# Kernel optimization log

Hardware: AMD Instinct MI355X
Metric: run time of the kernel (lower is better)

Reference implementation:

```python
import jax, jax.numpy as jnp
import numpy as np

N_NODES = 200000  # num_users + num_items
N_EDGES = 1000000
D = 64


def setup_inputs() -> dict:
    key = jax.random.key(0)
    ks = jax.random.split(key, 9)
    return {
        "src": jax.random.randint(ks[0], (N_EDGES,), 0, N_NODES, dtype=jnp.int32),
        "dst": jax.random.randint(ks[1], (N_EDGES,), 0, N_NODES, dtype=jnp.int32),
        "review_feat": jax.random.normal(ks[2], (N_EDGES, D), dtype=jnp.float32),
        "ci_r": jax.random.uniform(ks[3], (N_NODES, 1), dtype=jnp.float32),
        "feature": jax.random.normal(ks[4], (N_NODES, D), dtype=jnp.float32),
        "W1": jax.random.normal(ks[5], (D, D), dtype=jnp.float32) * 0.05,
        "W2": jax.random.normal(ks[6], (D, D), dtype=jnp.float32) * 0.05,
        "feature2": jax.random.normal(ks[7], (N_NODES, D), dtype=jnp.float32) * 0.05,
        "feature3": jax.random.normal(ks[8], (N_NODES, D), dtype=jnp.float32) * 0.05,
    }


def reference(src, dst, review_feat, ci_r, feature, W1, W2, feature2, feature3):
    # Eval-mode forward (is_training=False, freeze='', dropout = identity).
    # `feature` is assigned to g.srcdata['h_r'] in the original but never used.
    n = ci_r.shape[0]
    ci_src = ci_r[src]            # [E,1] gather of src norm coeff
    ci_dst = ci_r                 # [N,1]

    # Pass 1: edge linear on review features, scaled by src coeff, scatter-sum.
    r = review_feat @ W1.T                                   # [E,64]
    h1 = jax.ops.segment_sum(r * ci_src, dst, num_segments=n)
    rst_re = h1 * ci_dst

    # Pass 2: (src embedding + edge transform) messages.
    r_fe = review_feat @ W2.T                                # [E,64]
    m2 = (feature2[src] + r_fe) * ci_src
    h2 = jax.ops.segment_sum(m2, dst, num_segments=n)
    rst = h2 * ci_dst

    # Pass 3: pure src-embedding messages.
    m3 = feature3[src] * ci_src
    h3 = jax.ops.segment_sum(m3, dst, num_segments=n)
    rst_id = h3 * ci_dst

    return (rst, rst_re, rst_id)
```

## Files before the change

### kernel.cpp

```cpp
#include <hip/hip_runtime.h>

#define NN 200000
#define NE 1000000
#define DD 64
#define NCHUNK 196

typedef __bf16 bf16x4 __attribute__((ext_vector_type(4)));
typedef __bf16 bf16x8 __attribute__((ext_vector_type(8)));
typedef float  f32x4  __attribute__((ext_vector_type(4)));

static __device__ __forceinline__ bf16x8 pack8(const float* __restrict__ p) {
    float4 a = *reinterpret_cast<const float4*>(p);
    float4 b = *reinterpret_cast<const float4*>(p + 4);
    bf16x8 r;
    r[0] = (__bf16)a.x; r[1] = (__bf16)a.y; r[2] = (__bf16)a.z; r[3] = (__bf16)a.w;
    r[4] = (__bf16)b.x; r[5] = (__bf16)b.y; r[6] = (__bf16)b.z; r[7] = (__bf16)b.w;
    return r;
}

static __device__ __forceinline__ bf16x8 pack8s(const float* __restrict__ p, float c) {
    float4 a = *reinterpret_cast<const float4*>(p);
    float4 b = *reinterpret_cast<const float4*>(p + 4);
    bf16x8 r;
    r[0] = (__bf16)(a.x * c); r[1] = (__bf16)(a.y * c);
    r[2] = (__bf16)(a.z * c); r[3] = (__bf16)(a.w * c);
    r[4] = (__bf16)(b.x * c); r[5] = (__bf16)(b.y * c);
    r[6] = (__bf16)(b.z * c); r[7] = (__bf16)(b.w * c);
    return r;
}

__global__ __launch_bounds__(256) void k_prep(
    const int* __restrict__ dst, const float* __restrict__ f2,
    const float* __restrict__ f3, const float* __restrict__ ci,
    int* __restrict__ counts, __bf16* __restrict__ f2c, __bf16* __restrict__ f3c)
{
    const int b = blockIdx.x;
    if (b < 1024) {
        for (int e = b * 256 + threadIdx.x; e < NE; e += 1024 * 256)
            atomicAdd(&counts[dst[e]], 1);
    } else {
        const size_t per = (size_t)NN * DD / 8;
        const size_t stride = (size_t)(gridDim.x - 1024) * 256;
        for (size_t i = (size_t)(b - 1024) * 256 + threadIdx.x; i < per; i += stride) {
            const int row = (int)(i >> 3);
            const float c = ci[row];
            *reinterpret_cast<bf16x8*>(f2c + i * 8) = pack8s(f2 + i * 8, c);
            *reinterpret_cast<bf16x8*>(f3c + i * 8) = pack8s(f3 + i * 8, c);
        }
    }
}

__global__ __launch_bounds__(256) void k_chunk_sums(const int* __restrict__ counts,
                                                    int* __restrict__ csum) {
    const int b = blockIdx.x, tid = threadIdx.x;
    const int base = b * 1024 + tid * 4;
    int s = 0;
#pragma unroll
    for (int j = 0; j < 4; ++j) {
        const int i = base + j;
        if (i < NN) s += counts[i];
    }
#pragma unroll
    for (int d = 32; d > 0; d >>= 1) s += __shfl_down(s, d);
    __shared__ int wsum[4];
    if ((tid & 63) == 0) wsum[tid >> 6] = s;
    __syncthreads();
    if (tid == 0) csum[b] = wsum[0] + wsum[1] + wsum[2] + wsum[3];
}

__global__ void k_scan_chunks(const int* __restrict__ csum, int* __restrict__ cofs) {
    if (threadIdx.x == 0 && blockIdx.x == 0) {
        int acc = 0;
        for (int i = 0; i < NCHUNK; ++i) { cofs[i] = acc; acc += csum[i]; }
    }
}

__global__ __launch_bounds__(256) void k_chunk_scan(const int* __restrict__ counts,
                                                    const int* __restrict__ cofs,
                                                    int* __restrict__ offs,
                                                    int* __restrict__ cursor) {
    const int b = blockIdx.x, tid = threadIdx.x;
    const int lane = tid & 63, wv = tid >> 6;
    const int base = b * 1024 + tid * 4;
    int c[4];
#pragma unroll
    for (int j = 0; j < 4; ++j) {
        const int i = base + j;
        c[j] = (i < NN) ? counts[i] : 0;
    }
    const int ls = c[0] + c[1] + c[2] + c[3];
    int v = ls;
#pragma unroll
    for (int d = 1; d < 64; d <<= 1) {
        const int u = __shfl_up(v, d);
        if (lane >= d) v += u;
    }
    __shared__ int wsum[4];
    if (lane == 63) wsum[wv] = v;
    __syncthreads();
    int wbase = 0;
    for (int w = 0; w < wv; ++w) wbase += wsum[w];
    int excl = cofs[b] + wbase + (v - ls);
#pragma unroll
    for (int j = 0; j < 4; ++j) {
        const int i = base + j;
        if (i < NN) { offs[i] = excl; cursor[i] = excl; }
        excl += c[j];
    }
}

__global__ __launch_bounds__(256) void k_permfill_msg(
    const int* __restrict__ dst, const int* __restrict__ src,
    const float* __restrict__ ci, const float* __restrict__ review,
    int* __restrict__ cursor, __bf16* __restrict__ mrev, int* __restrict__ srcs)
{
    const int tid = threadIdx.x;
    const int l16 = tid & 15;
    const int e   = blockIdx.x * 16 + (tid >> 4);

    const int s = src[e];
    const float cs = ci[s];
    int pos = 0;
    if (l16 == 0) pos = atomicAdd(&cursor[dst[e]], 1);
    pos = __shfl(pos, tid & 48);

    const float4 r = *reinterpret_cast<const float4*>(review + (size_t)e * DD + l16 * 4);
    bf16x4 m;
    m[0] = (__bf16)(r.x * cs); m[1] = (__bf16)(r.y * cs);
    m[2] = (__bf16)(r.z * cs); m[3] = (__bf16)(r.w * cs);
    *reinterpret_cast<bf16x4*>(mrev + (size_t)pos * DD + l16 * 4) = m;
    if (l16 == 0) srcs[pos] = s;
}

__global__ __launch_bounds__(256) void k_pull_fused(
    const __bf16* __restrict__ mrev, const int* __restrict__ srcs,
    const int* __restrict__ offs, const int* __restrict__ counts,
    const float* __restrict__ ci,
    const __bf16* __restrict__ f2c, const __bf16* __restrict__ f3c,
    const float* __restrict__ W1, const float* __restrict__ W2,
    float* __restrict__ out_rst, float* __restrict__ out_re,
    float* __restrict__ out_id)
{
    __shared__ __bf16 At[16][64];
    __shared__ float  S2[16][64];

    const int tid = threadIdx.x;
    const int l16 = tid & 15;
    const int q   = tid >> 4;
    const int n   = blockIdx.x * 16 + q;

    const int beg = offs[n];
    const int cnt = counts[n];

    float4 ax0 = {0,0,0,0}, a20 = {0,0,0,0}, a30 = {0,0,0,0};
    float4 ax1 = {0,0,0,0}, a21 = {0,0,0,0}, a31 = {0,0,0,0};

    int k = 0;
    for (; k + 2 <= cnt; k += 2) {
        const int sa = srcs[beg + k];
        const int sb = srcs[beg + k + 1];
        const bf16x4 ma = *reinterpret_cast<const bf16x4*>(mrev + (size_t)(beg + k) * DD + l16 * 4);
        const bf16x4 mb = *reinterpret_cast<const bf16x4*>(mrev + (size_t)(beg + k + 1) * DD + l16 * 4);
        const bf16x4 p2a = *reinterpret_cast<const bf16x4*>(f2c + (size_t)sa * DD + l16 * 4);
        const bf16x4 p2b = *reinterpret_cast<const bf16x4*>(f2c + (size_t)sb * DD + l16 * 4);
        const bf16x4 p3a = *reinterpret_cast<const bf16x4*>(f3c + (size_t)sa * DD + l16 * 4);
        const bf16x4 p3b = *reinterpret_cast<const bf16x4*>(f3c + (size_t)sb * DD + l16 * 4);
        ax0.x += (float)ma[0]; ax0.y += (float)ma[1];
        ax0.z += (float)ma[2]; ax0.w += (float)ma[3];
        ax1.x += (float)mb[0]; ax1.y += (float)mb[1];
        ax1.z += (float)mb[2]; ax1.w += (float)mb[3];
        a20.x += (float)p2a[0]; a20.y += (float)p2a[1];
        a20.z += (float)p2a[2]; a20.w += (float)p2a[3];
        a21.x += (float)p2b[0]; a21.y += (float)p2b[1];
        a21.z += (float)p2b[2]; a21.w += (float)p2b[3];
        a30.x += (float)p3a[0]; a30.y += (float)p3a[1];
        a30.z += (float)p3a[2]; a30.w += (float)p3a[3];
        a31.x += (float)p3b[0]; a31.y += (float)p3b[1];
        a31.z += (float)p3b[2]; a31.w += (float)p3b[3];
    }
    if (k < cnt) {
        const int sa = srcs[beg + k];
        const bf16x4 ma = *reinterpret_cast<const bf16x4*>(mrev + (size_t)(beg + k) * DD + l16 * 4);
        const bf16x4 p2a = *reinterpret_cast<const bf16x4*>(f2c + (size_t)sa * DD + l16 * 4);
        const bf16x4 p3a = *reinterpret_cast<const bf16x4*>(f3c + (size_t)sa * DD + l16 * 4);
        ax0.x += (float)ma[0]; ax0.y += (float)ma[1];
        ax0.z += (float)ma[2]; ax0.w += (float)ma[3];
        a20.x += (float)p2a[0]; a20.y += (float)p2a[1];
        a20.z += (float)p2a[2]; a20.w += (float)p2a[3];
        a30.x += (float)p3a[0]; a30.y += (float)p3a[1];
        a30.z += (float)p3a[2]; a30.w += (float)p3a[3];
    }

    const float cid = ci[n];
    float4 ax = {ax0.x + ax1.x, ax0.y + ax1.y, ax0.z + ax1.z, ax0.w + ax1.w};
    float4 a2 = {a20.x + a21.x, a20.y + a21.y, a20.z + a21.z, a20.w + a21.w};
    float4 a3 = {a30.x + a31.x, a30.y + a31.y, a30.z + a31.z, a30.w + a31.w};

    float4 v3 = {a3.x * cid, a3.y * cid, a3.z * cid, a3.w * cid};
    *reinterpret_cast<float4*>(out_id + (size_t)n * DD + l16 * 4) = v3;

    bf16x4 hb;
    hb[0] = (__bf16)(ax.x * cid); hb[1] = (__bf16)(ax.y * cid);
    hb[2] = (__bf16)(ax.z * cid); hb[3] = (__bf16)(ax.w * cid);
    *reinterpret_cast<bf16x4*>(&At[q][l16 * 4]) = hb;
    float4 s2v = {a2.x * cid, a2.y * cid, a2.z * cid, a2.w * cid};
    *reinterpret_cast<float4*>(&S2[q][l16 * 4]) = s2v;
    __syncthreads();

    const int w  = tid >> 6;
    const int lq = (tid & 63) >> 4;
    bf16x8 w1f[2], w2f[2];
#pragma unroll
    for (int kk = 0; kk < 2; ++kk) {
        const int off = (w * 16 + l16) * DD + kk * 32 + lq * 8;
        w1f[kk] = pack8(W1 + off);
        w2f[kk] = pack8(W2 + off);
    }
    const bf16x8 a0 = *reinterpret_cast<const bf16x8*>(&At[l16][lq * 8]);
    const bf16x8 a1 = *reinterpret_cast<const bf16x8*>(&At[l16][lq * 8 + 32]);

    const f32x4 zero = {0.f, 0.f, 0.f, 0.f};
    f32x4 acc1 = zero, acc2 = zero;
    acc1 = __builtin_amdgcn_mfma_f32_16x16x32_bf16(a0, w1f[0], acc1, 0, 0, 0);
    acc1 = __builtin_amdgcn_mfma_f32_16x16x32_bf16(a1, w1f[1], acc1, 0, 0, 0);
    acc2 = __builtin_amdgcn_mfma_f32_16x16x32_bf16(a0, w2f[0], acc2, 0, 0, 0);
    acc2 = __builtin_amdgcn_mfma_f32_16x16x32_bf16(a1, w2f[1], acc2, 0, 0, 0);

    const int base = blockIdx.x * 16;
#pragma unroll
    for (int i = 0; i < 4; ++i) {
        const int row = lq * 4 + i;
        const size_t o = (size_t)(base + row) * DD + w * 16 + l16;
        out_re[o]  = acc1[i];
        out_rst[o] = acc2[i] + S2[row][w * 16 + l16];
    }
}

__global__ __launch_bounds__(256) void gcn_mfma_kernel(
    const int* __restrict__ src, const int* __restrict__ dst,
    const float* __restrict__ review, const float* __restrict__ ci,
    const float* __restrict__ W1, const float* __restrict__ W2,
    const float* __restrict__ f2, const float* __restrict__ f3,
    float* __restrict__ out)
{
    float* out_rst = out;
    float* out_re  = out + (size_t)NN * DD;
    float* out_id  = out + 2 * (size_t)NN * DD;
    const int lane = threadIdx.x & 63;
    const int l16  = lane & 15;
    const int lq   = lane >> 4;
    const int wid  = blockIdx.x * (blockDim.x >> 6) + (threadIdx.x >> 6);
    const int nw   = gridDim.x * (blockDim.x >> 6);

    bf16x8 w1f[4][2], w2f[4][2];
#pragma unroll
    for (int c = 0; c < 4; ++c)
#pragma unroll
        for (int kk = 0; kk < 2; ++kk) {
            const int off = (c * 16 + l16) * DD + kk * 32 + lq * 8;
            w1f[c][kk] = pack8(W1 + off);
            w2f[c][kk] = pack8(W2 + off);
        }
    const f32x4 zero = {0.f, 0.f, 0.f, 0.f};
    for (int t = wid; t < NE / 16; t += nw) {
        const int e0 = t * 16;
        const float* xr = review + (size_t)(e0 + l16) * DD + lq * 8;
        const bf16x8 a0 = pack8(xr);
        const bf16x8 a1 = pack8(xr + 32);
        f32x4 acc1[4], acc2[4];
#pragma unroll
        for (int c = 0; c < 4; ++c) { acc1[c] = zero; acc2[c] = zero; }
#pragma unroll
        for (int c = 0; c < 4; ++c) {
            acc1[c] = __builtin_amdgcn_mfma_f32_16x16x32_bf16(a0, w1f[c][0], acc1[c], 0, 0, 0);
            acc1[c] = __builtin_amdgcn_mfma_f32_16x16x32_bf16(a1, w1f[c][1], acc1[c], 0, 0, 0);
            acc2[c] = __builtin_amdgcn_mfma_f32_16x16x32_bf16(a0, w2f[c][0], acc2[c], 0, 0, 0);
            acc2[c] = __builtin_amdgcn_mfma_f32_16x16x32_bf16(a1, w2f[c][1], acc2[c], 0, 0, 0);
        }
        int sA[4], dA[4]; float cf[4];
#pragma unroll
        for (int i = 0; i < 4; ++i) {
            const int e = e0 + lq * 4 + i;
            sA[i] = src[e]; dA[i] = dst[e];
            cf[i] = ci[sA[i]] * ci[dA[i]];
        }
#pragma unroll
        for (int i = 0; i < 4; ++i) {
            const size_t so = (size_t)sA[i] * DD;
            const size_t dofs = (size_t)dA[i] * DD;
            const float c_ = cf[i];
#pragma unroll
            for (int c = 0; c < 4; ++c) {
                const int col = c * 16 + l16;
                atomicAdd(out_re  + dofs + col, acc1[c][i] * c_);
                atomicAdd(out_rst + dofs + col, (f2[so + col] + acc2[c][i]) * c_);
                atomicAdd(out_id  + dofs + col, f3[so + col] * c_);
            }
        }
    }
}

extern "C" void kernel_launch(void* const* d_in, const int* in_sizes, int n_in,
                              void* d_out, int out_size, void* d_ws, size_t ws_size,
                              hipStream_t stream) {
    const int*   src    = (const int*)d_in[0];
    const int*   dst    = (const int*)d_in[1];
    const float* review = (const float*)d_in[2];
    const float* ci     = (const float*)d_in[3];
    const float* W1     = (const float*)d_in[5];
    const float* W2     = (const float*)d_in[6];
    const float* f2     = (const float*)d_in[7];
    const float* f3     = (const float*)d_in[8];
    float* out = (float*)d_out;
    float* out_rst = out;
    float* out_re  = out + (size_t)NN * DD;
    float* out_id  = out + 2 * (size_t)NN * DD;

    const size_t NEED = sizeof(int) * ((size_t)3 * NN + 512 + NE) +
                        2 * sizeof(__bf16) * (size_t)NN * DD +
                        sizeof(__bf16) * (size_t)NE * DD;
    if (ws_size < NEED) {
        hipMemsetAsync(out, 0, (size_t)out_size * sizeof(float), stream);
        gcn_mfma_kernel<<<2048, 256, 0, stream>>>(src, dst, review, ci, W1, W2, f2, f3, out);
        return;
    }

    char* w = (char*)d_ws;
    int* counts = (int*)w;    w += (size_t)NN * 4;
    int* offs   = (int*)w;    w += (size_t)NN * 4;
    int* cursor = (int*)w;    w += (size_t)NN * 4;
    int* csum   = (int*)w;    w += 256 * 4;
    int* cofs   = (int*)w;    w += 256 * 4;
    int* srcs   = (int*)w;    w += (size_t)NE * 4;
    __bf16* f2c = (__bf16*)w; w += (size_t)NN * DD * 2;
    __bf16* f3c = (__bf16*)w; w += (size_t)NN * DD * 2;
    __bf16* mrev = (__bf16*)w;

    hipMemsetAsync(counts, 0, (size_t)NN * 4, stream);
    k_prep        <<<3072, 256, 0, stream>>>(dst, f2, f3, ci, counts, f2c, f3c);
    k_chunk_sums  <<<NCHUNK, 256, 0, stream>>>(counts, csum);
    k_scan_chunks <<<1, 64, 0, stream>>>(csum, cofs);
    k_chunk_scan  <<<NCHUNK, 256, 0, stream>>>(counts, cofs, offs, cursor);
    k_permfill_msg<<<NE / 16, 256, 0, stream>>>(dst, src, ci, review, cursor, mrev, srcs);
    k_pull_fused  <<<NN / 16, 256, 0, stream>>>(mrev, srcs, offs, counts, ci,
                                                f2c, f3c, W1, W2,
                                                out_rst, out_re, out_id);
}
```

Before: 318.3 us.

## Drop bf16 pre-scaled feature copies and gather fp32 features with per-edge coeff

Removes the prep pass that converted feature2/feature3 to ci-scaled bf16 copies. The pull kernel now gathers fp32 rows directly and applies the source coefficient, which is stored next to the src index as an int2 per sorted edge. The memset is replaced by a small zero kernel and the histogram gets its own kernel. This saves writing and reading the 2x25.6MB bf16 copies, but the random gathers in the pull kernel now move twice as many bytes per row and also read the coefficient per edge.

Measured after the change: 316.1 us. About the same (-0.7%).

```diff
diff --git a/kernel.cpp b/kernel.cpp
--- a/kernel.cpp
+++ b/kernel.cpp
@@ -18,36 +18,20 @@
     return r;
 }
 
-static __device__ __forceinline__ bf16x8 pack8s(const float* __restrict__ p, float c) {
-    float4 a = *reinterpret_cast<const float4*>(p);
-    float4 b = *reinterpret_cast<const float4*>(p + 4);
-    bf16x8 r;
-    r[0] = (__bf16)(a.x * c); r[1] = (__bf16)(a.y * c);
-    r[2] = (__bf16)(a.z * c); r[3] = (__bf16)(a.w * c);
-    r[4] = (__bf16)(b.x * c); r[5] = (__bf16)(b.y * c);
-    r[6] = (__bf16)(b.z * c); r[7] = (__bf16)(b.w * c);
-    return r;
-}
-
-__global__ __launch_bounds__(256) void k_prep(
-    const int* __restrict__ dst, const float* __restrict__ f2,
-    const float* __restrict__ f3, const float* __restrict__ ci,
-    int* __restrict__ counts, __bf16* __restrict__ f2c, __bf16* __restrict__ f3c)
-{
-    const int b = blockIdx.x;
-    if (b < 1024) {
-        for (int e = b * 256 + threadIdx.x; e < NE; e += 1024 * 256)
-            atomicAdd(&counts[dst[e]], 1);
+__global__ __launch_bounds__(256) void k_zero(int* __restrict__ counts) {
+    const int i = (blockIdx.x * 256 + threadIdx.x) * 4;
+    if (i + 3 < NN) {
+        *reinterpret_cast<int4*>(counts + i) = make_int4(0, 0, 0, 0);
     } else {
-        const size_t per = (size_t)NN * DD / 8;
-        const size_t stride = (size_t)(gridDim.x - 1024) * 256;
-        for (size_t i = (size_t)(b - 1024) * 256 + threadIdx.x; i < per; i += stride) {
-            const int row = (int)(i >> 3);
-            const float c = ci[row];
-            *reinterpret_cast<bf16x8*>(f2c + i * 8) = pack8s(f2 + i * 8, c);
-            *reinterpret_cast<bf16x8*>(f3c + i * 8) = pack8s(f3 + i * 8, c);
-        }
-    }
+        for (int j = i; j < NN; ++j) counts[j] = 0;
+    }
+}
+
+__global__ __launch_bounds__(256) void k_hist(const int* __restrict__ dst,
+                                              int* __restrict__ counts) {
+    for (int e = blockIdx.x * blockDim.x + threadIdx.x; e < NE;
+         e += gridDim.x * blockDim.x)
+        atomicAdd(&counts[dst[e]], 1);
 }
 
 __global__ __launch_bounds__(256) void k_chunk_sums(const int* __restrict__ counts,
@@ -112,7 +96,7 @@
 __global__ __launch_bounds__(256) void k_permfill_msg(
     const int* __restrict__ dst, const int* __restrict__ src,
     const float* __restrict__ ci, const float* __restrict__ review,
-    int* __restrict__ cursor, __bf16* __restrict__ mrev, int* __restrict__ srcs)
+    int* __restrict__ cursor, __bf16* __restrict__ mrev, int2* __restrict__ esrc)
 {
     const int tid = threadIdx.x;
     const int l16 = tid & 15;
@@ -129,14 +113,14 @@
     m[0] = (__bf16)(r.x * cs); m[1] = (__bf16)(r.y * cs);
     m[2] = (__bf16)(r.z * cs); m[3] = (__bf16)(r.w * cs);
     *reinterpret_cast<bf16x4*>(mrev + (size_t)pos * DD + l16 * 4) = m;
-    if (l16 == 0) srcs[pos] = s;
+    if (l16 == 0) esrc[pos] = make_int2(s, __float_as_int(cs));
 }
 
 __global__ __launch_bounds__(256) void k_pull_fused(
-    const __bf16* __restrict__ mrev, const int* __restrict__ srcs,
+    const __bf16* __restrict__ mrev, const int2* __restrict__ esrc,
     const int* __restrict__ offs, const int* __restrict__ counts,
     const float* __restrict__ ci,
-    const __bf16* __restrict__ f2c, const __bf16* __restrict__ f3c,
+    const float* __restrict__ f2, const float* __restrict__ f3,
     const float* __restrict__ W1, const float* __restrict__ W2,
     float* __restrict__ out_rst, float* __restrict__ out_re,
     float* __restrict__ out_id)
@@ -157,38 +141,41 @@
 
     int k = 0;
     for (; k + 2 <= cnt; k += 2) {
-        const int sa = srcs[beg + k];
-        const int sb = srcs[beg + k + 1];
+        const int2 ea = esrc[beg + k];
+        const int2 eb = esrc[beg + k + 1];
+        const float ca = __int_as_float(ea.y);
+        const float cb = __int_as_float(eb.y);
         const bf16x4 ma = *reinterpret_cast<const bf16x4*>(mrev + (size_t)(beg + k) * DD + l16 * 4);
         const bf16x4 mb = *reinterpret_cast<const bf16x4*>(mrev + (size_t)(beg + k + 1) * DD + l16 * 4);
-        const bf16x4 p2a = *reinterpret_cast<const bf16x4*>(f2c + (size_t)sa * DD + l16 * 4);
-        const bf16x4 p2b = *reinterpret_cast<const bf16x4*>(f2c + (size_t)sb * DD + l16 * 4);
-        const bf16x4 p3a = *reinterpret_cast<const bf16x4*>(f3c + (size_t)sa * DD + l16 * 4);
-        const bf16x4 p3b = *reinterpret_cast<const bf16x4*>(f3c + (size_t)sb * DD + l16 * 4);
+        const float4 p2a = *reinterpret_cast<const float4*>(f2 + (size_t)ea.x * DD + l16 * 4);
+        const float4 p2b = *reinterpret_cast<const float4*>(f2 + (size_t)eb.x * DD + l16 * 4);
+        const float4 p3a = *reinterpret_cast<const float4*>(f3 + (size_t)ea.x * DD + l16 * 4);
+        const float4 p3b = *reinterpret_cast<const float4*>(f3 + (size_t)eb.x * DD + l16 * 4);
         ax0.x += (float)ma[0]; ax0.y += (float)ma[1];
         ax0.z += (float)ma[2]; ax0.w += (float)ma[3];
         ax1.x += (float)mb[0]; ax1.y += (float)mb[1];
         ax1.z += (float)mb[2]; ax1.w += (float)mb[3];
-        a20.x += (float)p2a[0]; a20.y += (float)p2a[1];
-        a20.z += (float)p2a[2]; a20.w += (float)p2a[3];
-        a21.x += (float)p2b[0]; a21.y += (float)p2b[1];
-        a21.z += (float)p2b[2]; a21.w += (float)p2b[3];
-        a30.x += (float)p3a[0]; a30.y += (float)p3a[1];
-        a30.z += (float)p3a[2]; a30.w += (float)p3a[3];
-        a31.x += (float)p3b[0]; a31.y += (float)p3b[1];
-        a31.z += (float)p3b[2]; a31.w += (float)p3b[3];
+        a20.x = fmaf(p2a.x, ca, a20.x); a20.y = fmaf(p2a.y, ca, a20.y);
+        a20.z = fmaf(p2a.z, ca, a20.z); a20.w = fmaf(p2a.w, ca, a20.w);
+        a21.x = fmaf(p2b.x, cb, a21.x); a21.y = fmaf(p2b.y, cb, a21.y);
+        a21.z = fmaf(p2b.z, cb, a21.z); a21.w = fmaf(p2b.w, cb, a21.w);
+        a30.x = fmaf(p3a.x, ca, a30.x); a30.y = fmaf(p3a.y, ca, a30.y);
+        a30.z = fmaf(p3a.z, ca, a30.z); a30.w = fmaf(p3a.w, ca, a30.w);
+        a31.x = fmaf(p3b.x, cb, a31.x); a31.y = fmaf(p3b.y, cb, a31.y);
+        a31.z = fmaf(p3b.z, cb, a31.z); a31.w = fmaf(p3b.w, cb, a31.w);
     }
     if (k < cnt) {
-        const int sa = srcs[beg + k];
+        const int2 ea = esrc[beg + k];
+        const float ca = __int_as_float(ea.y);
         const bf16x4 ma = *reinterpret_cast<const bf16x4*>(mrev + (size_t)(beg + k) * DD + l16 * 4);
-        const bf16x4 p2a = *reinterpret_cast<const bf16x4*>(f2c + (size_t)sa * DD + l16 * 4);
-        const bf16x4 p3a = *reinterpret_cast<const bf16x4*>(f3c + (size_t)sa * DD + l16 * 4);
+        const float4 p2a = *reinterpret_cast<const float4*>(f2 + (size_t)ea.x * DD + l16 * 4);
+        const float4 p3a = *reinterpret_cast<const float4*>(f3 + (size_t)ea.x * DD + l16 * 4);
         ax0.x += (float)ma[0]; ax0.y += (float)ma[1];
         ax0.z += (float)ma[2]; ax0.w += (float)ma[3];
-        a20.x += (float)p2a[0]; a20.y += (float)p2a[1];
-        a20.z += (float)p2a[2]; a20.w += (float)p2a[3];
-        a30.x += (float)p3a[0]; a30.y += (float)p3a[1];
-        a30.z += (float)p3a[2]; a30.w += (float)p3a[3];
+        a20.x = fmaf(p2a.x, ca, a20.x); a20.y = fmaf(p2a.y, ca, a20.y);
+        a20.z = fmaf(p2a.z, ca, a20.z); a20.w = fmaf(p2a.w, ca, a20.w);
+        a30.x = fmaf(p3a.x, ca, a30.x); a30.y = fmaf(p3a.y, ca, a30.y);
+        a30.z = fmaf(p3a.z, ca, a30.z); a30.w = fmaf(p3a.w, ca, a30.w);
     }
 
     const float cid = ci[n];
@@ -316,8 +303,8 @@
     float* out_re  = out + (size_t)NN * DD;
     float* out_id  = out + 2 * (size_t)NN * DD;
 
-    const size_t NEED = sizeof(int) * ((size_t)3 * NN + 512 + NE) +
-                        2 * sizeof(__bf16) * (size_t)NN * DD +
+    const size_t NEED = sizeof(int) * ((size_t)3 * NN + 512) +
+                        sizeof(int2) * (size_t)NE +
                         sizeof(__bf16) * (size_t)NE * DD;
     if (ws_size < NEED) {
         hipMemsetAsync(out, 0, (size_t)out_size * sizeof(float), stream);
@@ -331,18 +318,16 @@
     int* cursor = (int*)w;    w += (size_t)NN * 4;
     int* csum   = (int*)w;    w += 256 * 4;
     int* cofs   = (int*)w;    w += 256 * 4;
-    int* srcs   = (int*)w;    w += (size_t)NE * 4;
-    __bf16* f2c = (__bf16*)w; w += (size_t)NN * DD * 2;
-    __bf16* f3c = (__bf16*)w; w += (size_t)NN * DD * 2;
+    int2* esrc  = (int2*)w;   w += (size_t)NE * 8;
     __bf16* mrev = (__bf16*)w;
 
-    hipMemsetAsync(counts, 0, (size_t)NN * 4, stream);
-    k_prep        <<<3072, 256, 0, stream>>>(dst, f2, f3, ci, counts, f2c, f3c);
+    k_zero        <<<(NN / 4 + 255) / 256, 256, 0, stream>>>(counts);
+    k_hist        <<<1024, 256, 0, stream>>>(dst, counts);
     k_chunk_sums  <<<NCHUNK, 256, 0, stream>>>(counts, csum);
     k_scan_chunks <<<1, 64, 0, stream>>>(csum, cofs);
     k_chunk_scan  <<<NCHUNK, 256, 0, stream>>>(counts, cofs, offs, cursor);
-    k_permfill_msg<<<NE / 16, 256, 0, stream>>>(dst, src, ci, review, cursor, mrev, srcs);
-    k_pull_fused  <<<NN / 16, 256, 0, stream>>>(mrev, srcs, offs, counts, ci,
-                                                f2c, f3c, W1, W2,
+    k_permfill_msg<<<NE / 16, 256, 0, stream>>>(dst, src, ci, review, cursor, mrev, esrc);
+    k_pull_fused  <<<NN / 16, 256, 0, stream>>>(mrev, esrc, offs, counts, ci,
+                                                f2, f3, W1, W2,
                                                 out_rst, out_re, out_id);
 }
```
